# Performance work log

Measured on AMD Instinct MI355X. Metric: run time of the kernel, lower is better.

Reference implementation:

```python
import jax, jax.numpy as jnp
import numpy as np

EMBED_DIM = 1024
NUM_HEADS = 16
HEAD_DIM = EMBED_DIM // NUM_HEADS
B, QL, CL = 2, 2048, 2048


def setup_inputs() -> dict:
    key = jax.random.key(0)
    ks = jax.random.split(key, 10)
    s = 1.0 / np.sqrt(EMBED_DIM)  # torch Linear default init scale (approx)
    inp = {
        "query": jax.random.normal(ks[0], (B, QL, EMBED_DIM), jnp.float32),
        "context": jax.random.normal(ks[1], (B, CL, EMBED_DIM), jnp.float32),
        "Wq": jax.random.normal(ks[2], (EMBED_DIM, EMBED_DIM), jnp.float32) * s,
        "bq": jnp.zeros((EMBED_DIM,), jnp.float32),
        "Wk": jax.random.normal(ks[3], (EMBED_DIM, EMBED_DIM), jnp.float32) * s,
        "bk": jnp.zeros((EMBED_DIM,), jnp.float32),
        "Wv": jax.random.normal(ks[4], (EMBED_DIM, EMBED_DIM), jnp.float32) * s,
        "bv": jnp.zeros((EMBED_DIM,), jnp.float32),
        "Wo": jax.random.normal(ks[5], (EMBED_DIM, EMBED_DIM), jnp.float32) * s,
        "bo": jnp.zeros((EMBED_DIM,), jnp.float32),
    }
    return inp


def reference(query, context, Wq, bq, Wk, bk, Wv, bv, Wo, bo):
    b, ql, _ = query.shape
    cl = context.shape[1]
    # projections (torch Linear: x @ W.T + b; here W stored as (in, out) so x @ W + b)
    Q = (query @ Wq + bq).reshape(b, ql, NUM_HEADS, HEAD_DIM).transpose(0, 2, 1, 3)
    K = (context @ Wk + bk).reshape(b, cl, NUM_HEADS, HEAD_DIM).transpose(0, 2, 1, 3)
    V = (context @ Wv + bv).reshape(b, cl, NUM_HEADS, HEAD_DIM).transpose(0, 2, 1, 3)
    # scores [b, h, ql, cl]
    scores = jnp.einsum("bhqd,bhkd->bhqk", Q, K) / np.sqrt(HEAD_DIM).astype(np.float32)
    probs = jax.nn.softmax(scores, axis=-1)
    # dropout=0.0 (eval): identity
    attended = jnp.einsum("bhqk,bhkd->bhqd", probs, V)
    attended = attended.transpose(0, 2, 1, 3).reshape(b, ql, EMBED_DIM)
    return attended @ Wo + bo
```

## Files before the change

### kernel.cpp

```cpp
#include <hip/hip_runtime.h>
#include <hip/hip_bf16.h>
#include <stdint.h>

#define EMBED 1024
#define NH 16
#define HD 64
#define BATCH 2
#define QLEN 2048
#define CLEN 2048

typedef short short8 __attribute__((ext_vector_type(8)));
typedef unsigned short ushort8v __attribute__((ext_vector_type(8)));
typedef float f32x4 __attribute__((ext_vector_type(4)));
typedef float f32x16 __attribute__((ext_vector_type(16)));
typedef uint32_t u32x4 __attribute__((ext_vector_type(4)));

#define QSCALE 0.18033688f

__device__ __forceinline__ void async_load16(const void* g, void* l) {
    __builtin_amdgcn_global_load_lds((const __attribute__((address_space(1))) void*)g,
                                     (__attribute__((address_space(3))) void*)l, 16, 0, 0);
}

__device__ __forceinline__ uint32_t pack2(float a, float b) {
    float2 f{a, b};
    __hip_bfloat162 t = __float22bfloat162_rn(f);
    uint32_t u;
    __builtin_memcpy(&u, &t, 4);
    return u;
}

__global__ void prep(const float* __restrict__ query, const float* __restrict__ context,
                     __hip_bfloat16* __restrict__ qbf, __hip_bfloat16* __restrict__ cbf,
                     const float* __restrict__ W0, const float* __restrict__ W1,
                     const float* __restrict__ W2, const float* __restrict__ W3,
                     __hip_bfloat16* __restrict__ T0, __hip_bfloat16* __restrict__ T1,
                     __hip_bfloat16* __restrict__ T2, __hip_bfloat16* __restrict__ T3) {
    const int y = blockIdx.y;
    const int tid = threadIdx.x;
    if (y < 2) {
        const float* src = y ? context : query;
        __hip_bfloat16* dst = y ? cbf : qbf;
#pragma unroll
        for (int k = 0; k < 4; k++) {
            const int i = (blockIdx.x * 1024 + k * 256 + tid) * 4;
            float4 v = *(const float4*)(src + i);
            __hip_bfloat16 h[4];
            h[0] = __float2bfloat16(v.x);
            h[1] = __float2bfloat16(v.y);
            h[2] = __float2bfloat16(v.z);
            h[3] = __float2bfloat16(v.w);
            *(ushort4*)(dst + i) = *(const ushort4*)h;
        }
    } else {
        const int z = y - 2;
        const float* W = z == 0 ? W0 : z == 1 ? W1 : z == 2 ? W2 : W3;
        __hip_bfloat16* Wt = z == 0 ? T0 : z == 1 ? T1 : z == 2 ? T2 : T3;
        __shared__ float t[32][33];
        const int tx = tid & 31, ty = tid >> 5;
        const int n0 = (blockIdx.x & 31) * 32, k0 = (blockIdx.x >> 5) * 32;
#pragma unroll
        for (int r = 0; r < 4; r++)
            t[ty * 4 + r][tx] = W[(size_t)(k0 + ty * 4 + r) * EMBED + n0 + tx];
        __syncthreads();
#pragma unroll
        for (int r = 0; r < 4; r++)
            Wt[(size_t)(n0 + ty * 4 + r) * EMBED + k0 + tx] = __float2bfloat16(t[tx][ty * 4 + r]);
    }
}

__device__ __forceinline__ void gemm128_acc(
    const __hip_bfloat16* __restrict__ A, const __hip_bfloat16* __restrict__ Bt,
    int m0, int n0, __hip_bfloat16* As, __hip_bfloat16* Bs, f32x4 acc[4][4]) {
    const int K = EMBED;
    const int tid = threadIdx.x;
    const int wave = __builtin_amdgcn_readfirstlane(tid >> 6);
    const int lane = tid & 63, l15 = lane & 15, quad = lane >> 4;
    const int wm = (wave >> 1) * 64, wn = (wave & 1) * 64;
    const int srow = tid >> 2, sseg = (tid & 3) * 8;
    for (int k0 = 0; k0 < K; k0 += 32) {
        __syncthreads();
#pragma unroll
        for (int s = 0; s < 2; s++) {
            async_load16(A + (size_t)(m0 + s * 64 + srow) * K + k0 + sseg,
                         As + (size_t)(s * 256 + wave * 64) * 8);
            async_load16(Bt + (size_t)(n0 + s * 64 + srow) * K + k0 + sseg,
                         Bs + (size_t)(s * 256 + wave * 64) * 8);
        }
        __syncthreads();
        short8 af[4], bf[4];
#pragma unroll
        for (int t = 0; t < 4; t++) {
            af[t] = *(const short8*)(As + (wm + t * 16 + l15) * 32 + quad * 8);
            bf[t] = *(const short8*)(Bs + (wn + t * 16 + l15) * 32 + quad * 8);
        }
#pragma unroll
        for (int mt = 0; mt < 4; mt++)
#pragma unroll
            for (int nt = 0; nt < 4; nt++)
                acc[mt][nt] = __builtin_amdgcn_mfma_f32_16x16x32_bf16(af[mt], bf[nt], acc[mt][nt], 0, 0, 0);
    }
}

__global__ __launch_bounds__(256, 3) void proj128(
    const __hip_bfloat16* __restrict__ qbf, const __hip_bfloat16* __restrict__ cbf,
    const __hip_bfloat16* __restrict__ Wqt, const __hip_bfloat16* __restrict__ Wkvt,
    const float* __restrict__ bq, const float* __restrict__ bk, const float* __restrict__ bv,
    __hip_bfloat16* __restrict__ Qp, __hip_bfloat16* __restrict__ Kp, __hip_bfloat16* __restrict__ Vtr) {
    __shared__ __hip_bfloat16 smem[8704];
    __hip_bfloat16* As = smem;
    __hip_bfloat16* Bs = smem + 4096;
    const int j = blockIdx.x;
    const int blk = (j & 7) * 96 + (j >> 3);
    const __hip_bfloat16 *A, *Bt;
    int m0, n0;
    if (blk < 256) {
        A = qbf; Bt = Wqt; m0 = (blk >> 3) * 128; n0 = (blk & 7) * 128;
    } else {
        const int f = blk - 256;
        A = cbf; Bt = Wkvt; m0 = (f >> 4) * 128; n0 = (f & 15) * 128;
    }
    f32x4 acc[4][4] = {};
    gemm128_acc(A, Bt, m0, n0, As, Bs, acc);

    const int tid = threadIdx.x;
    const int wave = __builtin_amdgcn_readfirstlane(tid >> 6);
    const int lane = tid & 63, l15 = lane & 15, quad = lane >> 4;
    const int wm = (wave >> 1) * 64, wn = (wave & 1) * 64;

    if (blk >= 256 && n0 >= 1024) {
        const int cb = n0 - 1024;
        const int b2 = m0 >> 11;
        const int tokb = m0 & 2047;
        __hip_bfloat16* T = smem;
#pragma unroll
        for (int hh = 0; hh < 2; hh++) {
            __syncthreads();
            if ((wn >> 6) == hh) {
#pragma unroll
                for (int nt = 0; nt < 4; nt++) {
                    const int cn = nt * 16 + l15;
                    const float bvv = bv[cb + hh * 64 + cn];
#pragma unroll
                    for (int mt = 0; mt < 4; mt++) {
                        const int m = wm + mt * 16 + quad * 4;
                        __hip_bfloat16 vb[4];
#pragma unroll
                        for (int r = 0; r < 4; r++) vb[r] = __float2bfloat16(acc[mt][nt][r] + bvv);
                        *(ushort4*)(T + cn * 136 + m) = *(const ushort4*)vb;
                    }
                }
            }
            __syncthreads();
            const int r = tid >> 2;
            const int seg = (tid & 3) * 32;
            unsigned short* dst = (unsigned short*)Vtr +
                (size_t)(b2 * 1024 + cb + hh * 64 + r) * CLEN + tokb + seg;
            const unsigned short* srcp = (const unsigned short*)(T + r * 136 + seg);
#pragma unroll
            for (int u = 0; u < 4; u++)
                *(ushort8v*)(dst + u * 8) = *(const ushort8v*)(srcp + u * 8);
        }
    } else {
        const bool isQ = (blk < 256);
        const float* bias = isQ ? bq : bk;
        __hip_bfloat16* C = isQ ? Qp : Kp;
        const float sc = isQ ? QSCALE : 1.0f;
#pragma unroll
        for (int mt = 0; mt < 4; mt++) {
#pragma unroll
            for (int nt = 0; nt < 4; nt++) {
                const int c = n0 + wn + nt * 16 + l15;
                const float bvv = bias[c];
                const int r0 = m0 + wm + mt * 16 + quad * 4;
#pragma unroll
                for (int r = 0; r < 4; r++)
                    C[(size_t)(r0 + r) * 1024 + c] = __float2bfloat16((acc[mt][nt][r] + bvv) * sc);
            }
        }
    }
}

__global__ __launch_bounds__(256, 4) void oproj(
    const __hip_bfloat16* __restrict__ A, const __hip_bfloat16* __restrict__ Bt,
    const float* __restrict__ bias, float* __restrict__ C) {
    __shared__ __hip_bfloat16 As[64 * 32];
    __shared__ __hip_bfloat16 Bs[128 * 32];
    const int K = EMBED, N = EMBED;
    const int j = blockIdx.x;
    const int L = (j & 7) * 64 + (j >> 3);
    const int m0 = (L >> 3) * 64, n0 = (L & 7) * 128;
    const int tid = threadIdx.x;
    const int wave = __builtin_amdgcn_readfirstlane(tid >> 6);
    const int lane = tid & 63, l15 = lane & 15, quad = lane >> 4;
    const int wm = (wave & 1) * 32, wn = (wave >> 1) * 64;
    const int srow = tid >> 2, sseg = (tid & 3) * 8;
    f32x4 acc[2][4] = {};
    for (int k0 = 0; k0 < K; k0 += 32) {
        __syncthreads();
        async_load16(A + (size_t)(m0 + srow) * K + k0 + sseg, As + (size_t)(wave * 64) * 8);
#pragma unroll
        for (int s = 0; s < 2; s++)
            async_load16(Bt + (size_t)(n0 + s * 64 + srow) * K + k0 + sseg,
                         Bs + (size_t)(s * 256 + wave * 64) * 8);
        __syncthreads();
        short8 af[2], bf[4];
#pragma unroll
        for (int t = 0; t < 2; t++)
            af[t] = *(const short8*)(As + (wm + t * 16 + l15) * 32 + quad * 8);
#pragma unroll
        for (int t = 0; t < 4; t++)
            bf[t] = *(const short8*)(Bs + (wn + t * 16 + l15) * 32 + quad * 8);
#pragma unroll
        for (int mt = 0; mt < 2; mt++)
#pragma unroll
            for (int nt = 0; nt < 4; nt++)
                acc[mt][nt] = __builtin_amdgcn_mfma_f32_16x16x32_bf16(af[mt], bf[nt], acc[mt][nt], 0, 0, 0);
    }
#pragma unroll
    for (int mt = 0; mt < 2; mt++) {
#pragma unroll
        for (int nt = 0; nt < 4; nt++) {
            const int c = n0 + wn + nt * 16 + l15;
            const float bvv = bias[c];
            const int r0 = m0 + wm + mt * 16 + quad * 4;
#pragma unroll
            for (int r = 0; r < 4; r++)
                C[(size_t)(r0 + r) * N + c] = acc[mt][nt][r] + bvv;
        }
    }
}

__global__ __launch_bounds__(256, 2) void flash_attn(
    const __hip_bfloat16* __restrict__ Q, const __hip_bfloat16* __restrict__ K,
    const __hip_bfloat16* __restrict__ Vt, __hip_bfloat16* __restrict__ O) {
    __shared__ __hip_bfloat16 Ks[2][128 * 64];
    __shared__ __hip_bfloat16 Vs[2][64 * 128];
    const int tid = threadIdx.x;
    const int wave = __builtin_amdgcn_readfirstlane(tid >> 6);
    const int lane = tid & 63, l31 = lane & 31, hbit = lane >> 5;
    const int j = blockIdx.x;
    const int L = (j & 7) * 64 + (j >> 3);
    const int hy = L >> 4;
    const int b = hy >> 4, h = hy & 15;
    const int q0 = (L & 15) * 128;
    const size_t kbase = (size_t)b * CLEN * EMBED + (size_t)h * HD;
    const size_t vtbase = (size_t)((b * NH + h) * HD) * CLEN;
    const int srow8 = lane >> 3;

    const __hip_bfloat16* qptr =
        Q + (size_t)(b * QLEN + q0 + wave * 32 + l31) * EMBED + h * HD + hbit * 8;
    short8 qf[4];
#pragma unroll
    for (int t = 0; t < 4; t++) qf[t] = *(const short8*)(qptr + t * 16);

    f32x16 o[2] = {};
    float lsA = 0.f, lsB = 0.f, lsC = 0.f, lsD = 0.f;

    const __hip_bfloat16* pk[4];
    const __hip_bfloat16* pv[4];
#pragma unroll
    for (int u = 0; u < 4; u++) {
        const int iK = wave * 4 + u;
        pk[u] = K + kbase + (size_t)(iK * 8 + srow8) * EMBED +
                (((lane & 7) ^ srow8 ^ (iK & 7)) * 8);
        const int dV = iK * 4 + (lane >> 4);
        const int rswV = (dV & 7) ^ ((dV >> 3) & 7);
        pv[u] = Vt + vtbase + (size_t)dV * CLEN + (((lane & 15) ^ rswV) * 8);
    }

#pragma unroll
    for (int u = 0; u < 4; u++) {
        const int iK = wave * 4 + u;
        async_load16(pk[u], Ks[0] + iK * 512);
        async_load16(pv[u], Vs[0] + iK * 512);
        pk[u] += (size_t)128 * EMBED;
        pv[u] += 128;
    }

    const int rsw0 = (l31 & 7) ^ (l31 >> 3);
    const int rsw1 = (l31 & 7) ^ (4 + (l31 >> 3));

    for (int t = 0; t < 16; ++t) {
        const int cur = t & 1;
        __syncthreads();
        if (t < 15) {
#pragma unroll
            for (int u = 0; u < 4; u++) {
                const int iK = wave * 4 + u;
                async_load16(pk[u], Ks[cur ^ 1] + iK * 512);
                async_load16(pv[u], Vs[cur ^ 1] + iK * 512);
                pk[u] += (size_t)128 * EMBED;
                pv[u] += 128;
            }
        }
        const __hip_bfloat16* stK = Ks[cur];
        const __hip_bfloat16* stV = Vs[cur];

#pragma unroll
        for (int hh = 0; hh < 2; hh++) {
            const __hip_bfloat16* kr0 = stK + (hh * 64 + l31) * 64;
            const __hip_bfloat16* kr1 = stK + (hh * 64 + 32 + l31) * 64;
            short8 kf[2][4];
#pragma unroll
            for (int kc = 0; kc < 4; kc++) {
                kf[0][kc] = *(const short8*)(kr0 + ((2 * kc + hbit) ^ rsw0) * 8);
                kf[1][kc] = *(const short8*)(kr1 + ((2 * kc + hbit) ^ rsw1) * 8);
            }
            f32x16 sv0 = {}, sv1 = {};
            __builtin_amdgcn_s_setprio(1);
#pragma unroll
            for (int kc = 0; kc < 4; kc++) {
                sv0 = __builtin_amdgcn_mfma_f32_32x32x16_bf16(kf[0][kc], qf[kc], sv0, 0, 0, 0);
                sv1 = __builtin_amdgcn_mfma_f32_32x32x16_bf16(kf[1][kc], qf[kc], sv1, 0, 0, 0);
            }
            __builtin_amdgcn_s_setprio(0);

            short8 vf[2][4];
#pragma unroll
            for (int dm = 0; dm < 2; dm++) {
                const int vsw = dm ? rsw1 : rsw0;
                const __hip_bfloat16* vr = stV + (dm * 32 + l31) * 128 + hh * 64;
#pragma unroll
                for (int k2 = 0; k2 < 4; k2++)
                    vf[dm][k2] = *(const short8*)(vr + ((2 * k2 + hbit) ^ vsw) * 8);
            }

            uint32_t dw[2][8];
#pragma unroll
            for (int i = 0; i < 8; i++) {
                const float a0 = __builtin_amdgcn_exp2f(sv0[2 * i]);
                const float a1 = __builtin_amdgcn_exp2f(sv0[2 * i + 1]);
                const float b0 = __builtin_amdgcn_exp2f(sv1[2 * i]);
                const float b1 = __builtin_amdgcn_exp2f(sv1[2 * i + 1]);
                if (i & 1) { lsB += a0 + a1; lsD += b0 + b1; }
                else       { lsA += a0 + a1; lsC += b0 + b1; }
                dw[0][i] = pack2(a0, a1);
                dw[1][i] = pack2(b0, b1);
            }

#pragma unroll
            for (int mc = 0; mc < 2; mc++) {
#pragma unroll
                for (int tp = 0; tp < 2; tp++) {
                    u32x4 fb;
#if __has_builtin(__builtin_amdgcn_permlane32_swap)
                    {
                        auto s02 = __builtin_amdgcn_permlane32_swap(dw[mc][4 * tp + 0], dw[mc][4 * tp + 2], false, false);
                        auto s13 = __builtin_amdgcn_permlane32_swap(dw[mc][4 * tp + 1], dw[mc][4 * tp + 3], false, false);
                        fb[0] = s02[0];
                        fb[1] = s13[0];
                        fb[2] = s02[1];
                        fb[3] = s13[1];
                    }
#else
                    {
                        const uint32_t a0 = hbit ? dw[mc][4 * tp + 2] : dw[mc][4 * tp + 0];
                        const uint32_t a1 = hbit ? dw[mc][4 * tp + 3] : dw[mc][4 * tp + 1];
                        const uint32_t b0 = hbit ? dw[mc][4 * tp + 0] : dw[mc][4 * tp + 2];
                        const uint32_t b1 = hbit ? dw[mc][4 * tp + 1] : dw[mc][4 * tp + 3];
                        const uint32_t x0 = (uint32_t)__shfl_xor((int)b0, 32);
                        const uint32_t x1 = (uint32_t)__shfl_xor((int)b1, 32);
                        fb[0] = hbit ? x0 : a0;
                        fb[1] = hbit ? x1 : a1;
                        fb[2] = hbit ? a0 : x0;
                        fb[3] = hbit ? a1 : x1;
                    }
#endif
                    const short8 pfr = __builtin_bit_cast(short8, fb);
                    const int kc2 = mc * 2 + tp;
                    __builtin_amdgcn_s_setprio(1);
                    o[0] = __builtin_amdgcn_mfma_f32_32x32x16_bf16(vf[0][kc2], pfr, o[0], 0, 0, 0);
                    o[1] = __builtin_amdgcn_mfma_f32_32x32x16_bf16(vf[1][kc2], pfr, o[1], 0, 0, 0);
                    __builtin_amdgcn_s_setprio(0);
                }
            }
        }
    }

    float lsum = (lsA + lsB) + (lsC + lsD);
    lsum += __shfl_xor(lsum, 32);
    const float inv = 1.0f / lsum;
    const int q = q0 + wave * 32 + l31;
    __hip_bfloat16* orow = O + (size_t)(b * QLEN + q) * EMBED + h * HD;
#pragma unroll
    for (int dm = 0; dm < 2; dm++) {
#pragma unroll
        for (int g = 0; g < 4; g++) {
            __hip_bfloat16 ob[4];
#pragma unroll
            for (int r = 0; r < 4; r++) ob[r] = __float2bfloat16(o[dm][g * 4 + r] * inv);
            *(ushort4*)(orow + dm * 32 + hbit * 4 + g * 8) = *(const ushort4*)ob;
        }
    }
}

extern "C" void kernel_launch(void* const* d_in, const int* in_sizes, int n_in,
                              void* d_out, int out_size, void* d_ws, size_t ws_size,
                              hipStream_t stream) {
    const float* query = (const float*)d_in[0];
    const float* context = (const float*)d_in[1];
    const float* Wq = (const float*)d_in[2];
    const float* bq = (const float*)d_in[3];
    const float* Wk = (const float*)d_in[4];
    const float* bk = (const float*)d_in[5];
    const float* Wv = (const float*)d_in[6];
    const float* bv = (const float*)d_in[7];
    const float* Wo = (const float*)d_in[8];
    const float* bo = (const float*)d_in[9];
    float* out = (float*)d_out;

    const int NTOK = BATCH * QLEN;
    const int NACT = NTOK * EMBED;
    const int NW = EMBED * EMBED;

    __hip_bfloat16* qbf = (__hip_bfloat16*)d_ws;
    __hip_bfloat16* cbf = qbf + NACT;
    __hip_bfloat16* Wqt = cbf + NACT;
    __hip_bfloat16* Wkt = Wqt + NW;
    __hip_bfloat16* Wvt = Wkt + NW;
    __hip_bfloat16* Wot = Wvt + NW;
    __hip_bfloat16* Qp = Wot + NW;
    __hip_bfloat16* Kp = Qp + NACT;
    __hip_bfloat16* Vtr = Kp + NACT;
    __hip_bfloat16* att = Vtr + NACT;

    prep<<<dim3(1024, 6), 256, 0, stream>>>(query, context, qbf, cbf,
                                            Wq, Wk, Wv, Wo, Wqt, Wkt, Wvt, Wot);

    proj128<<<768, 256, 0, stream>>>(qbf, cbf, Wqt, Wkt, bq, bk, bv, Qp, Kp, Vtr);

    flash_attn<<<512, 256, 0, stream>>>(Qp, Kp, Vtr, att);

    oproj<<<512, 256, 0, stream>>>(att, Wot, bo, out);
}
```

Measured before the change: 203.5 us.

## Shrink flash-attention tiles to 64 queries and 64 keys per block

```diff
diff --git a/kernel.cpp b/kernel.cpp
--- a/kernel.cpp
+++ b/kernel.cpp
@@ -231,22 +231,21 @@
     }
 }
 
-__global__ __launch_bounds__(256, 2) void flash_attn(
+__global__ __launch_bounds__(128, 2) void flash_attn(
     const __hip_bfloat16* __restrict__ Q, const __hip_bfloat16* __restrict__ K,
     const __hip_bfloat16* __restrict__ Vt, __hip_bfloat16* __restrict__ O) {
-    __shared__ __hip_bfloat16 Ks[2][128 * 64];
-    __shared__ __hip_bfloat16 Vs[2][64 * 128];
+    __shared__ __hip_bfloat16 Ks[2][64 * 64];
+    __shared__ __hip_bfloat16 Vs[2][64 * 64];
     const int tid = threadIdx.x;
     const int wave = __builtin_amdgcn_readfirstlane(tid >> 6);
     const int lane = tid & 63, l31 = lane & 31, hbit = lane >> 5;
     const int j = blockIdx.x;
-    const int L = (j & 7) * 64 + (j >> 3);
-    const int hy = L >> 4;
+    const int L = (j & 7) * 128 + (j >> 3);
+    const int hy = L >> 5;
     const int b = hy >> 4, h = hy & 15;
-    const int q0 = (L & 15) * 128;
+    const int q0 = (L & 31) * 64;
     const size_t kbase = (size_t)b * CLEN * EMBED + (size_t)h * HD;
     const size_t vtbase = (size_t)((b * NH + h) * HD) * CLEN;
-    const int srow8 = lane >> 3;
 
     const __hip_bfloat16* qptr =
         Q + (size_t)(b * QLEN + q0 + wave * 32 + l31) * EMBED + h * HD + hbit * 8;
@@ -257,123 +256,116 @@
     f32x16 o[2] = {};
     float lsA = 0.f, lsB = 0.f, lsC = 0.f, lsD = 0.f;
 
+    const int srow = tid >> 3;
+    const int sg = tid & 7;
     const __hip_bfloat16* pk[4];
     const __hip_bfloat16* pv[4];
 #pragma unroll
     for (int u = 0; u < 4; u++) {
-        const int iK = wave * 4 + u;
-        pk[u] = K + kbase + (size_t)(iK * 8 + srow8) * EMBED +
-                (((lane & 7) ^ srow8 ^ (iK & 7)) * 8);
-        const int dV = iK * 4 + (lane >> 4);
-        const int rswV = (dV & 7) ^ ((dV >> 3) & 7);
-        pv[u] = Vt + vtbase + (size_t)dV * CLEN + (((lane & 15) ^ rswV) * 8);
+        const int row = u * 16 + srow;
+        const int rsw = (row & 7) ^ (row >> 3);
+        pk[u] = K + kbase + (size_t)row * EMBED + ((sg ^ rsw) * 8);
+        pv[u] = Vt + vtbase + (size_t)row * CLEN + ((sg ^ rsw) * 8);
     }
 
 #pragma unroll
     for (int u = 0; u < 4; u++) {
-        const int iK = wave * 4 + u;
-        async_load16(pk[u], Ks[0] + iK * 512);
-        async_load16(pv[u], Vs[0] + iK * 512);
-        pk[u] += (size_t)128 * EMBED;
-        pv[u] += 128;
+        async_load16(pk[u], Ks[0] + u * 1024 + tid * 8);
+        async_load16(pv[u], Vs[0] + u * 1024 + tid * 8);
+        pk[u] += (size_t)64 * EMBED;
+        pv[u] += 64;
     }
 
     const int rsw0 = (l31 & 7) ^ (l31 >> 3);
     const int rsw1 = (l31 & 7) ^ (4 + (l31 >> 3));
 
-    for (int t = 0; t < 16; ++t) {
+    for (int t = 0; t < 32; ++t) {
         const int cur = t & 1;
         __syncthreads();
-        if (t < 15) {
+        if (t < 31) {
 #pragma unroll
             for (int u = 0; u < 4; u++) {
-                const int iK = wave * 4 + u;
-                async_load16(pk[u], Ks[cur ^ 1] + iK * 512);
-                async_load16(pv[u], Vs[cur ^ 1] + iK * 512);
-                pk[u] += (size_t)128 * EMBED;
-                pv[u] += 128;
+                async_load16(pk[u], Ks[cur ^ 1] + u * 1024 + tid * 8);
+                async_load16(pv[u], Vs[cur ^ 1] + u * 1024 + tid * 8);
+                pk[u] += (size_t)64 * EMBED;
+                pv[u] += 64;
             }
         }
         const __hip_bfloat16* stK = Ks[cur];
         const __hip_bfloat16* stV = Vs[cur];
 
-#pragma unroll
-        for (int hh = 0; hh < 2; hh++) {
-            const __hip_bfloat16* kr0 = stK + (hh * 64 + l31) * 64;
-            const __hip_bfloat16* kr1 = stK + (hh * 64 + 32 + l31) * 64;
-            short8 kf[2][4];
-#pragma unroll
-            for (int kc = 0; kc < 4; kc++) {
-                kf[0][kc] = *(const short8*)(kr0 + ((2 * kc + hbit) ^ rsw0) * 8);
-                kf[1][kc] = *(const short8*)(kr1 + ((2 * kc + hbit) ^ rsw1) * 8);
-            }
-            f32x16 sv0 = {}, sv1 = {};
-            __builtin_amdgcn_s_setprio(1);
-#pragma unroll
-            for (int kc = 0; kc < 4; kc++) {
-                sv0 = __builtin_amdgcn_mfma_f32_32x32x16_bf16(kf[0][kc], qf[kc], sv0, 0, 0, 0);
-                sv1 = __builtin_amdgcn_mfma_f32_32x32x16_bf16(kf[1][kc], qf[kc], sv1, 0, 0, 0);
-            }
-            __builtin_amdgcn_s_setprio(0);
-
-            short8 vf[2][4];
-#pragma unroll
-            for (int dm = 0; dm < 2; dm++) {
-                const int vsw = dm ? rsw1 : rsw0;
-                const __hip_bfloat16* vr = stV + (dm * 32 + l31) * 128 + hh * 64;
-#pragma unroll
-                for (int k2 = 0; k2 < 4; k2++)
-                    vf[dm][k2] = *(const short8*)(vr + ((2 * k2 + hbit) ^ vsw) * 8);
-            }
-
-            uint32_t dw[2][8];
-#pragma unroll
-            for (int i = 0; i < 8; i++) {
-                const float a0 = __builtin_amdgcn_exp2f(sv0[2 * i]);
-                const float a1 = __builtin_amdgcn_exp2f(sv0[2 * i + 1]);
-                const float b0 = __builtin_amdgcn_exp2f(sv1[2 * i]);
-                const float b1 = __builtin_amdgcn_exp2f(sv1[2 * i + 1]);
-                if (i & 1) { lsB += a0 + a1; lsD += b0 + b1; }
-                else       { lsA += a0 + a1; lsC += b0 + b1; }
-                dw[0][i] = pack2(a0, a1);
-                dw[1][i] = pack2(b0, b1);
-            }
-
-#pragma unroll
-            for (int mc = 0; mc < 2; mc++) {
-#pragma unroll
-                for (int tp = 0; tp < 2; tp++) {
-                    u32x4 fb;
+        short8 kf[2][4];
+#pragma unroll
+        for (int kc = 0; kc < 4; kc++) {
+            kf[0][kc] = *(const short8*)(stK + l31 * 64 + ((2 * kc + hbit) ^ rsw0) * 8);
+            kf[1][kc] = *(const short8*)(stK + (32 + l31) * 64 + ((2 * kc + hbit) ^ rsw1) * 8);
+        }
+        f32x16 sv0 = {}, sv1 = {};
+        __builtin_amdgcn_s_setprio(1);
+#pragma unroll
+        for (int kc = 0; kc < 4; kc++) {
+            sv0 = __builtin_amdgcn_mfma_f32_32x32x16_bf16(kf[0][kc], qf[kc], sv0, 0, 0, 0);
+            sv1 = __builtin_amdgcn_mfma_f32_32x32x16_bf16(kf[1][kc], qf[kc], sv1, 0, 0, 0);
+        }
+        __builtin_amdgcn_s_setprio(0);
+
+        short8 vf[2][4];
+#pragma unroll
+        for (int dm = 0; dm < 2; dm++) {
+            const int vsw = dm ? rsw1 : rsw0;
+            const __hip_bfloat16* vr = stV + (dm * 32 + l31) * 64;
+#pragma unroll
+            for (int k2 = 0; k2 < 4; k2++)
+                vf[dm][k2] = *(const short8*)(vr + ((2 * k2 + hbit) ^ vsw) * 8);
+        }
+
+        uint32_t dw[2][8];
+#pragma unroll
+        for (int i = 0; i < 8; i++) {
+            const float a0 = __builtin_amdgcn_exp2f(sv0[2 * i]);
+            const float a1 = __builtin_amdgcn_exp2f(sv0[2 * i + 1]);
+            const float b0 = __builtin_amdgcn_exp2f(sv1[2 * i]);
+            const float b1 = __builtin_amdgcn_exp2f(sv1[2 * i + 1]);
+            if (i & 1) { lsB += a0 + a1; lsD += b0 + b1; }
+            else       { lsA += a0 + a1; lsC += b0 + b1; }
+            dw[0][i] = pack2(a0, a1);
+            dw[1][i] = pack2(b0, b1);
+        }
+
+#pragma unroll
+        for (int mc = 0; mc < 2; mc++) {
+#pragma unroll
+            for (int tp = 0; tp < 2; tp++) {
+                u32x4 fb;
 #if __has_builtin(__builtin_amdgcn_permlane32_swap)
-                    {
-                        auto s02 = __builtin_amdgcn_permlane32_swap(dw[mc][4 * tp + 0], dw[mc][4 * tp + 2], false, false);
-                        auto s13 = __builtin_amdgcn_permlane32_swap(dw[mc][4 * tp + 1], dw[mc][4 * tp + 3], false, false);
-                        fb[0] = s02[0];
-                        fb[1] = s13[0];
-                        fb[2] = s02[1];
-                        fb[3] = s13[1];
-                    }
+                {
+                    auto s02 = __builtin_amdgcn_permlane32_swap(dw[mc][4 * tp + 0], dw[mc][4 * tp + 2], false, false);
+                    auto s13 = __builtin_amdgcn_permlane32_swap(dw[mc][4 * tp + 1], dw[mc][4 * tp + 3], false, false);
+                    fb[0] = s02[0];
+                    fb[1] = s13[0];
+                    fb[2] = s02[1];
+                    fb[3] = s13[1];
+                }
 #else
-                    {
-                        const uint32_t a0 = hbit ? dw[mc][4 * tp + 2] : dw[mc][4 * tp + 0];
-                        const uint32_t a1 = hbit ? dw[mc][4 * tp + 3] : dw[mc][4 * tp + 1];
-                        const uint32_t b0 = hbit ? dw[mc][4 * tp + 0] : dw[mc][4 * tp + 2];
-                        const uint32_t b1 = hbit ? dw[mc][4 * tp + 1] : dw[mc][4 * tp + 3];
-                        const uint32_t x0 = (uint32_t)__shfl_xor((int)b0, 32);
-                        const uint32_t x1 = (uint32_t)__shfl_xor((int)b1, 32);
-                        fb[0] = hbit ? x0 : a0;
-                        fb[1] = hbit ? x1 : a1;
-                        fb[2] = hbit ? a0 : x0;
-                        fb[3] = hbit ? a1 : x1;
-                    }
+                {
+                    const uint32_t a0 = hbit ? dw[mc][4 * tp + 2] : dw[mc][4 * tp + 0];
+                    const uint32_t a1 = hbit ? dw[mc][4 * tp + 3] : dw[mc][4 * tp + 1];
+                    const uint32_t b0 = hbit ? dw[mc][4 * tp + 0] : dw[mc][4 * tp + 2];
+                    const uint32_t b1 = hbit ? dw[mc][4 * tp + 1] : dw[mc][4 * tp + 3];
+                    const uint32_t x0 = (uint32_t)__shfl_xor((int)b0, 32);
+                    const uint32_t x1 = (uint32_t)__shfl_xor((int)b1, 32);
+                    fb[0] = hbit ? x0 : a0;
+                    fb[1] = hbit ? x1 : a1;
+                    fb[2] = hbit ? a0 : x0;
+                    fb[3] = hbit ? a1 : x1;
+                }
 #endif
-                    const short8 pfr = __builtin_bit_cast(short8, fb);
-                    const int kc2 = mc * 2 + tp;
-                    __builtin_amdgcn_s_setprio(1);
-                    o[0] = __builtin_amdgcn_mfma_f32_32x32x16_bf16(vf[0][kc2], pfr, o[0], 0, 0, 0);
-                    o[1] = __builtin_amdgcn_mfma_f32_32x32x16_bf16(vf[1][kc2], pfr, o[1], 0, 0, 0);
-                    __builtin_amdgcn_s_setprio(0);
-                }
+                const short8 pfr = __builtin_bit_cast(short8, fb);
+                const int kc2 = mc * 2 + tp;
+                __builtin_amdgcn_s_setprio(1);
+                o[0] = __builtin_amdgcn_mfma_f32_32x32x16_bf16(vf[0][kc2], pfr, o[0], 0, 0, 0);
+                o[1] = __builtin_amdgcn_mfma_f32_32x32x16_bf16(vf[1][kc2], pfr, o[1], 0, 0, 0);
+                __builtin_amdgcn_s_setprio(0);
             }
         }
     }
@@ -430,7 +422,7 @@
 
     proj128<<<768, 256, 0, stream>>>(qbf, cbf, Wqt, Wkt, bq, bk, bv, Qp, Kp, Vtr);
 
-    flash_attn<<<512, 256, 0, stream>>>(Qp, Kp, Vtr, att);
+    flash_attn<<<1024, 128, 0, stream>>>(Qp, Kp, Vtr, att);
 
     oproj<<<512, 256, 0, stream>>>(att, Wot, bo, out);
 }
```

Measured after the change: 213.1 us. 4.7% more time.
